# Kernel optimization log

Hardware: AMD Instinct MI355X
Metric: run time of the kernel (lower is better)

Reference implementation:

```python
import jax, jax.numpy as jnp
from jax import lax
import numpy as np

# ---- init hyperparameters (from init_kwargs) ----
STRIDE = 1
DP_CHANNELS = 1
ATOM_R = 8
ATOM_C = 8
NUMB_ATOM = 128
T_SC = 3
K = 256
BATCH = 32
IMG = 64


def setup_inputs() -> dict:
    key = jax.random.key(0)
    k1, k2 = jax.random.split(key)
    Y = jax.random.normal(k1, (BATCH, DP_CHANNELS, IMG, IMG), dtype=jnp.float32)
    # ConvTranspose2d weight layout: (numb_atom, dp_channels, atom_c, atom_r)
    W = jax.random.normal(k2, (NUMB_ATOM, DP_CHANNELS, ATOM_C, ATOM_R), dtype=jnp.float32)
    # normalise_weights(): each (i, j) filter divided by its L2 norm
    W = W / jnp.sqrt(jnp.sum(W ** 2, axis=(2, 3), keepdims=True))
    return {"Y": Y, "W_D": W}


def _conv_D(X, W):
    # PyTorch ConvTranspose2d (stride=1, no padding): full convolution with
    # spatially-flipped kernel; W is (in=numb_atom, out=dp_channels, kh, kw).
    kh, kw = W.shape[2], W.shape[3]
    return lax.conv_general_dilated(
        X, jnp.flip(W, (2, 3)), (1, 1),
        [(kh - 1, kh - 1), (kw - 1, kw - 1)],
        dimension_numbers=('NCHW', 'IOHW', 'NCHW'))


def _conv_Dt(R, Wt):
    # PyTorch Conv2d (VALID, stride=1): Wt is (out=numb_atom, in=dp, kh, kw)
    return lax.conv_general_dilated(
        R, Wt, (1, 1), 'VALID', dimension_numbers=('NCHW', 'OIHW', 'NCHW'))


def _hard_threshold_k(X, k):
    # keep the k largest-|.| entries per sample (over flattened C,H,W)
    B = X.shape[0]
    flat = X.reshape(B, -1)
    _, idx = lax.top_k(jnp.abs(flat), k)                      # [B, k]
    vals = jnp.take_along_axis(flat, idx, axis=1)             # [B, k]
    out = jnp.zeros_like(flat).at[jnp.arange(B)[:, None], idx].set(vals)
    return out.reshape(X.shape)


def _linesearch(Y, X, W, Wt, k):
    R = Y - _conv_D(X, W)
    g = _conv_Dt(R, Wt)
    l2_start = jnp.sum(R ** 2)

    def attempt(alpha):
        Xu = _hard_threshold_k(X + alpha * g, k)
        err = jnp.sum((Y - _conv_D(Xu, W)) ** 2)
        return Xu, err

    Xu0, err0 = attempt(jnp.float32(1.0))

    def cond(s):
        _, _, err, count = s
        return (err >= l2_start) & (count <= 15)

    def body(s):
        alpha, _, _, count = s
        alpha = alpha * jnp.float32(0.5)
        Xu, err = attempt(alpha)
        return (alpha, Xu, err, count + 1)

    alpha, Xu, err, _ = lax.while_loop(
        cond, body, (jnp.float32(1.0), Xu0, err0, jnp.int32(0)))
    return Xu, err, alpha


def reference(Y, W_D):
    # D_trans.weight = D.weight.permute(0,1,3,2) -> (numb_atom, dp, atom_r, atom_c)
    Wt = jnp.swapaxes(W_D, 2, 3)
    kh, kw = Wt.shape[2], Wt.shape[3]
    B, _, H, W_sp = Y.shape
    X = jnp.zeros((B, W_D.shape[0], H - kh + 1, W_sp - kw + 1), dtype=Y.dtype)
    for _ in range(T_SC):
        X, _, _ = _linesearch(Y, X, W_D, Wt, K)
    return X
```

## Files before the change

### kernel.cpp

```cpp
#include <hip/hip_runtime.h>
#include <stdint.h>

#define NB   32
#define NCH  128
#define IMG  64
#define IMG2 4096
#define OH   57
#define OHW  3249
#define CHW  415872
#define KTOP 256
#define NATT 17
#define NS   32
#define SCAP 512
#define NCAP 1536
#define NBUCK 8192
#define HSHIFT 18
#define TGT  512
#define RSTRIDE 72
#define NZB  257
#define BMW  12996

typedef unsigned long long ull;

__global__ void k_init(int* support_cnt) {
    if (threadIdx.x < NB) support_cnt[threadIdx.x] = 0;
}

__global__ __launch_bounds__(256) void k_resid(
    const float* __restrict__ Y, const float* __restrict__ W,
    const int* __restrict__ support_cnt, const uint32_t* __restrict__ support_idx,
    const float* __restrict__ support_val, float* __restrict__ Rg, double* __restrict__ l2part,
    uint32_t* __restrict__ hist, int* __restrict__ cand_cnt)
{
    int bx = blockIdx.x, tid = threadIdx.x;
    if (bx >= NB) {
        int zb = bx - NB;
        if (zb < 256) {
            ((uint4*)hist)[zb * 256 + tid] = make_uint4(0u, 0u, 0u, 0u);
        } else {
            ((uint4*)cand_cnt)[tid] = make_uint4(0u, 0u, 0u, 0u);
        }
        return;
    }
    int b = bx;
    __shared__ float Rs[IMG2];
    const float4* Y4 = (const float4*)(Y + b * IMG2);
    float4* R4 = (float4*)Rs;
    for (int i = tid; i < IMG2 / 4; i += 256) R4[i] = Y4[i];
    __syncthreads();
    int n = support_cnt[b];
    for (int task = tid; task < n * 64; task += 256) {
        int i = task >> 6, tap = task & 63, p = tap >> 3, q = tap & 7;
        uint32_t idx = support_idx[b * KTOP + i];
        float val = support_val[b * KTOP + i];
        int c = idx / OHW, rem = idx % OHW, s = rem / OH, t = rem % OH;
        float w = W[c * 64 + p * 8 + q];
        atomicAdd(&Rs[(s + p) * IMG + (t + q)], -val * w);
    }
    __syncthreads();
    double acc = 0.0;
    for (int i = tid; i < IMG2; i += 256) {
        float v = Rs[i];
        Rg[b * IMG2 + i] = v;
        acc += (double)v * (double)v;
    }
    __shared__ double red[256];
    red[tid] = acc; __syncthreads();
    for (int s2 = 128; s2 > 0; s2 >>= 1) { if (tid < s2) red[tid] += red[tid + s2]; __syncthreads(); }
    if (tid == 0) l2part[b] = red[0];
}

__global__ __launch_bounds__(256) void k_conv(
    const float* __restrict__ Rg, const float* __restrict__ W,
    float* __restrict__ g_out, uint32_t* __restrict__ hist)
{
    int b = blockIdx.x, cg0 = blockIdx.y, tid = threadIdx.x;
    __shared__ float Rs[71 * 72];
    __shared__ uint32_t hl[NBUCK];
    for (int i = tid; i < 71 * 72; i += 256) Rs[i] = 0.f;
    for (int i = tid; i < NBUCK; i += 256) hl[i] = 0u;
    __syncthreads();
    const float4* R4 = (const float4*)(Rg + b * IMG2);
    for (int i = tid; i < 1024; i += 256) {
        int row = i >> 4, col4 = (i & 15) * 4;
        *(float4*)&Rs[row * 72 + col4] = R4[i];
    }
    __syncthreads();
    int csub = tid >> 7;
    int tile = tid & 127;
    bool active = tile < 120;
    int tr = active ? tile / 15 : 0;
    int tc = active ? tile % 15 : 0;
    int s0 = tr * 8, t0 = tc * 4;

    for (int sub = 0; sub < 4; ++sub) {
        int c = cg0 * 8 + sub * 2 + csub;
        int c_s = __builtin_amdgcn_readfirstlane(c);
        const float* Wc = W + c_s * 64;

        float acc[8][4];
#pragma unroll
        for (int r = 0; r < 8; ++r)
#pragma unroll
            for (int cc = 0; cc < 4; ++cc) acc[r][cc] = 0.f;

#pragma unroll
        for (int rho = 0; rho < 15; ++rho) {
            float rb[12];
            const float* rp = &Rs[(s0 + rho) * 72 + t0];
            *(float4*)&rb[0] = *(const float4*)rp;
            *(float4*)&rb[4] = *(const float4*)(rp + 4);
            *(float4*)&rb[8] = *(const float4*)(rp + 8);
#pragma unroll
            for (int r = 0; r < 8; ++r) {
                const int p = rho - r;
                if (p >= 0 && p < 8) {
#pragma unroll
                    for (int q = 0; q < 8; ++q) {
                        float wv = Wc[q * 8 + p];
#pragma unroll
                        for (int cc = 0; cc < 4; ++cc)
                            acc[r][cc] = fmaf(rb[cc + q], wv, acc[r][cc]);
                    }
                }
            }
        }
        if (active) {
            float* go = g_out + (size_t)(b * NCH + c) * OHW;
#pragma unroll
            for (int r = 0; r < 8; ++r) {
                int s = s0 + r;
                if (s < OH) {
#pragma unroll
                    for (int cc = 0; cc < 4; ++cc) {
                        int t = t0 + cc;
                        if (t < OH) {
                            float v = acc[r][cc];
                            go[s * OH + t] = v;
                            uint32_t bits = __float_as_uint(v) & 0x7fffffffu;
                            atomicAdd(&hl[bits >> HSHIFT], 1u);
                        }
                    }
                }
            }
        }
    }
    __syncthreads();
    for (int i = tid; i < NBUCK; i += 256) {
        uint32_t v = hl[i];
        if (v) atomicAdd(&hist[b * NBUCK + i], v);
    }
}

__global__ __launch_bounds__(256) void k_thresh(const uint32_t* __restrict__ hist,
                                                uint32_t* __restrict__ thr) {
    int b = blockIdx.x, tid = threadIdx.x;
    uint32_t h[32];
    uint32_t s = 0;
    const uint32_t* hb = hist + b * NBUCK + tid * 32;
#pragma unroll
    for (int k = 0; k < 32; ++k) { h[k] = hb[k]; s += h[k]; }
    __shared__ uint32_t buf[2][256];
    int cur = 0;
    buf[0][tid] = s;
    __syncthreads();
    for (int d = 1; d < 256; d <<= 1) {
        uint32_t v = buf[cur][tid];
        if (tid + d < 256) v += buf[cur][tid + d];
        buf[cur ^ 1][tid] = v;
        cur ^= 1;
        __syncthreads();
    }
    uint32_t sufme = buf[cur][tid];
    uint32_t base  = (tid < 255) ? buf[cur][tid + 1] : 0u;
    if (tid == 0 && buf[cur][0] < TGT) thr[b] = 0u;
    if (base < TGT && sufme >= TGT) {
        uint32_t acc = base; int bk = 0;
#pragma unroll
        for (int k = 31; k >= 0; --k) {
            acc += h[k];
            if (acc >= TGT) { bk = tid * 32 + k; break; }
        }
        thr[b] = (uint32_t)bk << HSHIFT;
    }
}

__global__ __launch_bounds__(256) void k_collect(
    const float* __restrict__ g, const uint32_t* __restrict__ thr,
    int* __restrict__ cand_cnt, uint32_t* __restrict__ cand_idx, float* __restrict__ cand_g)
{
    int b = blockIdx.y;
    int i4 = blockIdx.x * 256 + threadIdx.x;
    if (i4 >= CHW / 4) return;
    int slice = blockIdx.x & (NS - 1);
    uint32_t tb = thr[b];
    float4 v4 = ((const float4*)(g + (size_t)b * CHW))[i4];
    float vv[4] = { v4.x, v4.y, v4.z, v4.w };
#pragma unroll
    for (int k = 0; k < 4; ++k) {
        uint32_t bits = __float_as_uint(vv[k]) & 0x7fffffffu;
        if (bits >= tb) {
            int pos = atomicAdd(&cand_cnt[b * NS + slice], 1);
            if (pos < SCAP) {
                cand_idx[(b * NS + slice) * SCAP + pos] = (uint32_t)(i4 * 4 + k);
                cand_g[(b * NS + slice) * SCAP + pos] = vv[k];
            }
        }
    }
}

__global__ __launch_bounds__(1024) void k_suppg(
    const float* __restrict__ g,
    const int* __restrict__ support_cnt, const uint32_t* __restrict__ support_idx,
    const int* __restrict__ cand_cnt, const uint32_t* __restrict__ cand_idx,
    const float* __restrict__ cand_g,
    uint32_t* __restrict__ ns_idx, float* __restrict__ ns_g, uint32_t* __restrict__ ns_pk,
    float* __restrict__ sup_g, uint32_t* __restrict__ sup_pk)
{
    int b = blockIdx.x, tid = threadIdx.x, lane = tid & 63;
    __shared__ uint32_t bm[BMW];
    __shared__ int cnts[NS];
    __shared__ ull ck[NCAP];
    __shared__ float cg_l[NCAP];
    __shared__ int nns_sh;
    int n = support_cnt[b];
    for (int i = tid; i < BMW / 4; i += 1024) ((uint4*)bm)[i] = make_uint4(0u, 0u, 0u, 0u);
    if (tid < NS) cnts[tid] = min(cand_cnt[b * NS + tid], SCAP);
    if (tid == 0) nns_sh = 0;
    __syncthreads();
    if (tid < KTOP) {
        if (tid < n) {
            uint32_t idx = support_idx[b * KTOP + tid];
            atomicOr(&bm[idx >> 5], 1u << (idx & 31));
            float gv = g[(size_t)b * CHW + idx];
            sup_g[b * KTOP + tid] = gv;
            int c = idx / OHW, r = idx % OHW, s = r / OH, t = r % OH;
            sup_pk[b * KTOP + tid] = (uint32_t)((c << 12) | (s << 6) | t);
        } else {
            sup_g[b * KTOP + tid] = 0.f;
            sup_pk[b * KTOP + tid] = 0u;
        }
    }
    __syncthreads();
    for (int t0 = tid; t0 < NS * SCAP; t0 += 1024) {
        int s = t0 >> 9, j = t0 & (SCAP - 1);
        bool keep = false; uint32_t idx = 0; float gv = 0.f;
        if (j < cnts[s]) {
            idx = cand_idx[(b * NS + s) * SCAP + j];
            gv = cand_g[(b * NS + s) * SCAP + j];
            keep = ((bm[idx >> 5] >> (idx & 31)) & 1u) == 0u;
        }
        ull mk = __ballot(keep);
        if (mk) {
            int basep = 0;
            if (lane == 0) basep = atomicAdd(&nns_sh, (int)__popcll(mk));
            basep = __shfl(basep, 0, 64);
            if (keep) {
                int p = basep + (int)__popcll(mk & ((1ull << lane) - 1ull));
                if (p < NCAP) {
                    ck[p] = ((ull)(__float_as_uint(gv) & 0x7fffffffu) << 32) | (ull)(uint32_t)(~idx);
                    cg_l[p] = gv;
                }
            }
        }
    }
    __syncthreads();
    int nns = min(nns_sh, NCAP);
    int nns8 = (nns + 7) & ~7;
    for (int i = nns + tid; i < nns8; i += 1024) ck[i] = 0ull;
    __syncthreads();
    ull myk[2]; int myr[2];
#pragma unroll
    for (int q = 0; q < 2; ++q) { int i = tid + 1024 * q; myk[q] = (i < nns) ? ck[i] : 0ull; myr[q] = 0; }
    for (int j = 0; j < nns8; j += 8) {
        ull t0 = ck[j], t1 = ck[j+1], t2 = ck[j+2], t3 = ck[j+3];
        ull t4 = ck[j+4], t5 = ck[j+5], t6 = ck[j+6], t7 = ck[j+7];
#pragma unroll
        for (int q = 0; q < 2; ++q) {
            myr[q] += ((t0 > myk[q]) ? 1 : 0) + ((t1 > myk[q]) ? 1 : 0)
                    + ((t2 > myk[q]) ? 1 : 0) + ((t3 > myk[q]) ? 1 : 0)
                    + ((t4 > myk[q]) ? 1 : 0) + ((t5 > myk[q]) ? 1 : 0)
                    + ((t6 > myk[q]) ? 1 : 0) + ((t7 > myk[q]) ? 1 : 0);
        }
    }
#pragma unroll
    for (int q = 0; q < 2; ++q) {
        int i = tid + 1024 * q;
        if (i < nns && myr[q] < KTOP) {
            uint32_t idx = ~(uint32_t)myk[q];
            int r = myr[q];
            ns_idx[b * KTOP + r] = idx;
            ns_g[b * KTOP + r] = cg_l[i];
            int c = idx / OHW, rr = idx % OHW, s = rr / OH, t = rr % OH;
            ns_pk[b * KTOP + r] = (uint32_t)((c << 12) | (s << 6) | t);
        }
    }
}

__global__ __launch_bounds__(1024) void k_att2(
    const float* __restrict__ Y, const float* __restrict__ W,
    const int* __restrict__ support_cnt, const uint32_t* __restrict__ support_idx,
    const float* __restrict__ support_val,
    const float* __restrict__ sup_g, const uint32_t* __restrict__ sup_pk,
    const uint32_t* __restrict__ ns_idx, const float* __restrict__ ns_g,
    const uint32_t* __restrict__ ns_pk,
    uint32_t* __restrict__ sel_idx, float* __restrict__ sel_val, double* __restrict__ err)
{
    int a = blockIdx.x, b = blockIdx.y, tid = threadIdx.x;
    int lane = tid & 63, wid = tid >> 6;
    float alpha = ldexpf(1.f, -a);
    int n = support_cnt[b];

    __shared__ float Wlds[NCH * 64];
    __shared__ float recon[64 * RSTRIDE];
    __shared__ ull kA[KTOP];
    __shared__ ull kB[KTOP];
    __shared__ float s_v[KTOP];
    __shared__ uint32_t s_pk2[KTOP];
    __shared__ double redd[16];

    uint32_t nsi = 0, pk_ns = 0, spi = 0, pk_sup = 0;
    float v_ns = 0.f, v_sup = 0.f;
    ull k_ns = 0, k_sup = 0;
    if (wid < 4) {
        nsi = ns_idx[b * KTOP + tid];
        v_ns = alpha * ns_g[b * KTOP + tid];
        pk_ns = ns_pk[b * KTOP + tid];
        k_ns = ((ull)(__float_as_uint(v_ns) & 0x7fffffffu) << 32) | (ull)(uint32_t)(~nsi);
        kA[tid] = k_ns;
        if (tid < n) {
            spi = support_idx[b * KTOP + tid];
            v_sup = fmaf(alpha, sup_g[b * KTOP + tid], support_val[b * KTOP + tid]);
            pk_sup = sup_pk[b * KTOP + tid];
        } else {
            spi = (uint32_t)(CHW + tid);
            v_sup = 0.f; pk_sup = 0u;
        }
        k_sup = ((ull)(__float_as_uint(v_sup) & 0x7fffffffu) << 32) | (ull)(uint32_t)(~spi);
        kB[tid] = k_sup;
    }
    __syncthreads();

    if (wid < 4) {
        int cb_ns = 0, cb_sup = 0;
        for (int j = 0; j < KTOP; j += 8) {
            ull t0 = kB[j], t1 = kB[j+1], t2 = kB[j+2], t3 = kB[j+3];
            ull t4 = kB[j+4], t5 = kB[j+5], t6 = kB[j+6], t7 = kB[j+7];
            cb_ns  += ((t0 > k_ns) ? 1 : 0) + ((t1 > k_ns) ? 1 : 0)
                    + ((t2 > k_ns) ? 1 : 0) + ((t3 > k_ns) ? 1 : 0)
                    + ((t4 > k_ns) ? 1 : 0) + ((t5 > k_ns) ? 1 : 0)
                    + ((t6 > k_ns) ? 1 : 0) + ((t7 > k_ns) ? 1 : 0);
            cb_sup += ((t0 > k_sup) ? 1 : 0) + ((t1 > k_sup) ? 1 : 0)
                    + ((t2 > k_sup) ? 1 : 0) + ((t3 > k_sup) ? 1 : 0)
                    + ((t4 > k_sup) ? 1 : 0) + ((t5 > k_sup) ? 1 : 0)
                    + ((t6 > k_sup) ? 1 : 0) + ((t7 > k_sup) ? 1 : 0);
        }
        int rank_ns = tid + cb_ns;
        int lo = 0, hi = KTOP;
        while (lo < hi) { int mid = (lo + hi) >> 1; if (kA[mid] > k_sup) lo = mid + 1; else hi = mid; }
        int rank_sup = lo + cb_sup;
        size_t o = ((size_t)a * NB + b) * KTOP;
        if (rank_ns < KTOP) {
            s_v[rank_ns] = v_ns; s_pk2[rank_ns] = pk_ns;
            sel_idx[o + rank_ns] = nsi; sel_val[o + rank_ns] = v_ns;
        }
        if (rank_sup < KTOP) {
            s_v[rank_sup] = v_sup; s_pk2[rank_sup] = pk_sup;
            sel_idx[o + rank_sup] = spi; sel_val[o + rank_sup] = v_sup;
        }
    } else {
        for (int i = tid - 256; i < 64 * RSTRIDE; i += 768) recon[i] = 0.f;
        for (int i = tid - 256; i < (NCH * 64) / 4; i += 768)
            ((float4*)Wlds)[i] = ((const float4*)W)[i];
    }
    __syncthreads();

    for (int task = tid; task < KTOP * 64; task += 1024) {
        int i = task >> 6, tap = task & 63, p = tap >> 3, q = tap & 7;
        uint32_t pk = s_pk2[i];
        float val = s_v[i];
        int c = pk >> 12, s = (pk >> 6) & 63, t = pk & 63;
        atomicAdd(&recon[(s + p) * RSTRIDE + (t + q)], val * Wlds[c * 64 + tap]);
    }
    __syncthreads();

    float4 y4 = ((const float4*)(Y + b * IMG2))[tid];
    int row = tid >> 4, col = (tid & 15) * 4;
    const float* rr = &recon[row * RSTRIDE + col];
    double accd = 0.0;
    float d0 = y4.x - rr[0]; accd += (double)d0 * (double)d0;
    float d1 = y4.y - rr[1]; accd += (double)d1 * (double)d1;
    float d2 = y4.z - rr[2]; accd += (double)d2 * (double)d2;
    float d3 = y4.w - rr[3]; accd += (double)d3 * (double)d3;
    for (int d = 32; d > 0; d >>= 1) accd += __shfl_xor(accd, d, 64);
    if (lane == 0) redd[wid] = accd;
    __syncthreads();
    if (tid == 0) {
        double e = 0.0;
#pragma unroll
        for (int w2 = 0; w2 < 16; ++w2) e += redd[w2];
        err[a * NB + b] = e;
    }
}

__global__ __launch_bounds__(256) void k_update(
    const double* __restrict__ l2part, const double* __restrict__ err,
    const uint32_t* __restrict__ sel_idx, const float* __restrict__ sel_val,
    int* __restrict__ support_cnt, uint32_t* __restrict__ support_idx, float* __restrict__ support_val)
{
    int b = blockIdx.x, tid = threadIdx.x;
    __shared__ double esum[NATT + 1];
    __shared__ int sel_sh;
    if (tid < NATT) {
        double e = 0.0;
        for (int b2 = 0; b2 < NB; ++b2) e += err[tid * NB + b2];
        esum[tid] = e;
    } else if (tid == NATT) {
        double l2 = 0.0;
        for (int b2 = 0; b2 < NB; ++b2) l2 += l2part[b2];
        esum[NATT] = l2;
    }
    __syncthreads();
    if (tid == 0) {
        double l2 = esum[NATT];
        int sel = NATT - 1;
        for (int a2 = 0; a2 < NATT; ++a2) if (esum[a2] < l2) { sel = a2; break; }
        sel_sh = sel;
    }
    __syncthreads();
    int a = sel_sh;
    __shared__ uint32_t ki[KTOP];
    __shared__ float kv[KTOP];
    ki[tid] = sel_idx[((size_t)a * NB + b) * KTOP + tid];
    kv[tid] = sel_val[((size_t)a * NB + b) * KTOP + tid];
    __syncthreads();
    uint32_t me = ki[tid];
    int rank = 0;
    for (int j = 0; j < KTOP; j += 8) {
        uint32_t a0 = ki[j], a1 = ki[j+1], a2 = ki[j+2], a3 = ki[j+3];
        uint32_t a4 = ki[j+4], a5 = ki[j+5], a6 = ki[j+6], a7 = ki[j+7];
        rank += ((a0 < me) ? 1 : 0) + ((a1 < me) ? 1 : 0) + ((a2 < me) ? 1 : 0) + ((a3 < me) ? 1 : 0)
              + ((a4 < me) ? 1 : 0) + ((a5 < me) ? 1 : 0) + ((a6 < me) ? 1 : 0) + ((a7 < me) ? 1 : 0);
    }
    support_idx[b * KTOP + rank] = me;
    support_val[b * KTOP + rank] = kv[tid];
    if (tid == 0) support_cnt[b] = KTOP;
}

__global__ void k_outzero(float4* __restrict__ out) {
    int i = blockIdx.x * 256 + threadIdx.x;
    if (i < (NB * CHW) / 4) out[i] = make_float4(0.f, 0.f, 0.f, 0.f);
}

__global__ void k_scatter(const uint32_t* __restrict__ support_idx, const float* __restrict__ support_val,
                          float* __restrict__ out) {
    int b = blockIdx.x, tid = threadIdx.x;
    if (tid < KTOP) out[(size_t)b * CHW + support_idx[b * KTOP + tid]] = support_val[b * KTOP + tid];
}

static size_t align256(size_t x) { return (x + 255) & ~(size_t)255; }

extern "C" void kernel_launch(void* const* d_in, const int* in_sizes, int n_in,
                              void* d_out, int out_size, void* d_ws, size_t ws_size,
                              hipStream_t stream)
{
    const float* Y = (const float*)d_in[0];
    const float* W = (const float*)d_in[1];
    float* out = (float*)d_out;

    char* p = (char*)d_ws;
    size_t off = 0;
    auto carve = [&](size_t bytes) { void* r = p + off; off = align256(off + bytes); return r; };
    float*    Rg          = (float*)   carve(NB * IMG2 * sizeof(float));
    uint32_t* hist        = (uint32_t*)carve((size_t)NB * NBUCK * sizeof(uint32_t));
    uint32_t* thr         = (uint32_t*)carve(NB * sizeof(uint32_t));
    int*      cand_cnt    = (int*)     carve(NB * NS * sizeof(int));
    double*   l2part      = (double*)  carve(NB * sizeof(double));
    double*   err         = (double*)  carve(NATT * NB * sizeof(double));
    int*      support_cnt = (int*)     carve(NB * sizeof(int));
    uint32_t* support_idx = (uint32_t*)carve(NB * KTOP * sizeof(uint32_t));
    float*    support_val = (float*)   carve(NB * KTOP * sizeof(float));
    uint32_t* sel_idx     = (uint32_t*)carve((size_t)NATT * NB * KTOP * sizeof(uint32_t));
    float*    sel_val     = (float*)   carve((size_t)NATT * NB * KTOP * sizeof(float));
    uint32_t* cand_idx    = (uint32_t*)carve((size_t)NB * NS * SCAP * sizeof(uint32_t));
    float*    cand_g      = (float*)   carve((size_t)NB * NS * SCAP * sizeof(float));
    uint32_t* ns_idx      = (uint32_t*)carve(NB * KTOP * sizeof(uint32_t));
    float*    ns_gbuf     = (float*)   carve(NB * KTOP * sizeof(float));
    uint32_t* ns_pk       = (uint32_t*)carve(NB * KTOP * sizeof(uint32_t));
    float*    sup_gbuf    = (float*)   carve(NB * KTOP * sizeof(float));
    uint32_t* sup_pk      = (uint32_t*)carve(NB * KTOP * sizeof(uint32_t));
    (void)ws_size; (void)in_sizes; (void)n_in; (void)out_size;

    k_init<<<1, 64, 0, stream>>>(support_cnt);
    for (int t = 0; t < 3; ++t) {
        k_resid<<<NB + NZB, 256, 0, stream>>>(Y, W, support_cnt, support_idx, support_val,
                                              Rg, l2part, hist, cand_cnt);
        k_conv<<<dim3(NB, 16), 256, 0, stream>>>(Rg, W, out, hist);
        k_thresh<<<NB, 256, 0, stream>>>(hist, thr);
        k_collect<<<dim3((CHW / 4 + 255) / 256, NB), 256, 0, stream>>>(out, thr, cand_cnt, cand_idx, cand_g);
        k_suppg<<<NB, 1024, 0, stream>>>(out, support_cnt, support_idx,
                                         cand_cnt, cand_idx, cand_g,
                                         ns_idx, ns_gbuf, ns_pk, sup_gbuf, sup_pk);
        k_att2<<<dim3(NATT, NB), 1024, 0, stream>>>(Y, W, support_cnt, support_idx, support_val,
                                                    sup_gbuf, sup_pk, ns_idx, ns_gbuf, ns_pk,
                                                    sel_idx, sel_val, err);
        k_update<<<NB, 256, 0, stream>>>(l2part, err, sel_idx, sel_val,
                                         support_cnt, support_idx, support_val);
    }
    k_outzero<<<((NB * CHW) / 4 + 255) / 256, 256, 0, stream>>>((float4*)out);
    k_scatter<<<NB, 256, 0, stream>>>(support_idx, support_val, out);
}
```

Baseline: 671.4 us.

## Shrink k_att2 to 512 threads, drop LDS weight copy, rebalance merge work

Restructures the attempt-evaluation kernel to 512 threads. Each thread now ranks one candidate: the first 256 take the new-support entries and the rest take the existing support entries, replacing the scheme where 4 waves each ranked two entries while the other waves idled. The 32KB shared-memory copy of the weights is removed and the scatter reads W straight from global memory (cached). This lowers LDS use and block size so more blocks can be resident per CU. The cost is that the atomic scatter and the final error reduction now run with half as many threads.

```diff
diff --git a/kernel.cpp b/kernel.cpp
--- a/kernel.cpp
+++ b/kernel.cpp
@@ -297,7 +297,7 @@
     }
 }
 
-__global__ __launch_bounds__(1024) void k_att2(
+__global__ __launch_bounds__(512) void k_att2(
     const float* __restrict__ Y, const float* __restrict__ W,
     const int* __restrict__ support_cnt, const uint32_t* __restrict__ support_idx,
     const float* __restrict__ support_val,
@@ -311,94 +311,92 @@
     float alpha = ldexpf(1.f, -a);
     int n = support_cnt[b];
 
-    __shared__ float Wlds[NCH * 64];
     __shared__ float recon[64 * RSTRIDE];
     __shared__ ull kA[KTOP];
     __shared__ ull kB[KTOP];
     __shared__ float s_v[KTOP];
     __shared__ uint32_t s_pk2[KTOP];
-    __shared__ double redd[16];
-
-    uint32_t nsi = 0, pk_ns = 0, spi = 0, pk_sup = 0;
-    float v_ns = 0.f, v_sup = 0.f;
-    ull k_ns = 0, k_sup = 0;
-    if (wid < 4) {
-        nsi = ns_idx[b * KTOP + tid];
-        v_ns = alpha * ns_g[b * KTOP + tid];
-        pk_ns = ns_pk[b * KTOP + tid];
-        k_ns = ((ull)(__float_as_uint(v_ns) & 0x7fffffffu) << 32) | (ull)(uint32_t)(~nsi);
-        kA[tid] = k_ns;
-        if (tid < n) {
-            spi = support_idx[b * KTOP + tid];
-            v_sup = fmaf(alpha, sup_g[b * KTOP + tid], support_val[b * KTOP + tid]);
-            pk_sup = sup_pk[b * KTOP + tid];
+    __shared__ double redd[8];
+
+    uint32_t myi = 0, mypk = 0;
+    float myv = 0.f;
+    ull myk = 0;
+    if (tid < KTOP) {
+        myi = ns_idx[b * KTOP + tid];
+        myv = alpha * ns_g[b * KTOP + tid];
+        mypk = ns_pk[b * KTOP + tid];
+        myk = ((ull)(__float_as_uint(myv) & 0x7fffffffu) << 32) | (ull)(uint32_t)(~myi);
+        kA[tid] = myk;
+    } else {
+        int t2 = tid - KTOP;
+        if (t2 < n) {
+            myi = support_idx[b * KTOP + t2];
+            myv = fmaf(alpha, sup_g[b * KTOP + t2], support_val[b * KTOP + t2]);
+            mypk = sup_pk[b * KTOP + t2];
         } else {
-            spi = (uint32_t)(CHW + tid);
-            v_sup = 0.f; pk_sup = 0u;
-        }
-        k_sup = ((ull)(__float_as_uint(v_sup) & 0x7fffffffu) << 32) | (ull)(uint32_t)(~spi);
-        kB[tid] = k_sup;
-    }
-    __syncthreads();
-
-    if (wid < 4) {
-        int cb_ns = 0, cb_sup = 0;
-        for (int j = 0; j < KTOP; j += 8) {
-            ull t0 = kB[j], t1 = kB[j+1], t2 = kB[j+2], t3 = kB[j+3];
-            ull t4 = kB[j+4], t5 = kB[j+5], t6 = kB[j+6], t7 = kB[j+7];
-            cb_ns  += ((t0 > k_ns) ? 1 : 0) + ((t1 > k_ns) ? 1 : 0)
-                    + ((t2 > k_ns) ? 1 : 0) + ((t3 > k_ns) ? 1 : 0)
-                    + ((t4 > k_ns) ? 1 : 0) + ((t5 > k_ns) ? 1 : 0)
-                    + ((t6 > k_ns) ? 1 : 0) + ((t7 > k_ns) ? 1 : 0);
-            cb_sup += ((t0 > k_sup) ? 1 : 0) + ((t1 > k_sup) ? 1 : 0)
-                    + ((t2 > k_sup) ? 1 : 0) + ((t3 > k_sup) ? 1 : 0)
-                    + ((t4 > k_sup) ? 1 : 0) + ((t5 > k_sup) ? 1 : 0)
-                    + ((t6 > k_sup) ? 1 : 0) + ((t7 > k_sup) ? 1 : 0);
-        }
-        int rank_ns = tid + cb_ns;
+            myi = (uint32_t)(CHW + t2);
+            myv = 0.f; mypk = 0u;
+        }
+        myk = ((ull)(__float_as_uint(myv) & 0x7fffffffu) << 32) | (ull)(uint32_t)(~myi);
+        kB[t2] = myk;
+    }
+    for (int i = tid; i < 64 * RSTRIDE; i += 512) recon[i] = 0.f;
+    __syncthreads();
+
+    int cb = 0;
+    for (int j = 0; j < KTOP; j += 8) {
+        ull t0 = kB[j], t1 = kB[j+1], t2 = kB[j+2], t3 = kB[j+3];
+        ull t4 = kB[j+4], t5 = kB[j+5], t6 = kB[j+6], t7 = kB[j+7];
+        cb += ((t0 > myk) ? 1 : 0) + ((t1 > myk) ? 1 : 0)
+            + ((t2 > myk) ? 1 : 0) + ((t3 > myk) ? 1 : 0)
+            + ((t4 > myk) ? 1 : 0) + ((t5 > myk) ? 1 : 0)
+            + ((t6 > myk) ? 1 : 0) + ((t7 > myk) ? 1 : 0);
+    }
+    int rank;
+    if (tid < KTOP) {
+        rank = tid + cb;
+    } else {
         int lo = 0, hi = KTOP;
-        while (lo < hi) { int mid = (lo + hi) >> 1; if (kA[mid] > k_sup) lo = mid + 1; else hi = mid; }
-        int rank_sup = lo + cb_sup;
-        size_t o = ((size_t)a * NB + b) * KTOP;
-        if (rank_ns < KTOP) {
-            s_v[rank_ns] = v_ns; s_pk2[rank_ns] = pk_ns;
-            sel_idx[o + rank_ns] = nsi; sel_val[o + rank_ns] = v_ns;
-        }
-        if (rank_sup < KTOP) {
-            s_v[rank_sup] = v_sup; s_pk2[rank_sup] = pk_sup;
-            sel_idx[o + rank_sup] = spi; sel_val[o + rank_sup] = v_sup;
-        }
-    } else {
-        for (int i = tid - 256; i < 64 * RSTRIDE; i += 768) recon[i] = 0.f;
-        for (int i = tid - 256; i < (NCH * 64) / 4; i += 768)
-            ((float4*)Wlds)[i] = ((const float4*)W)[i];
-    }
-    __syncthreads();
-
-    for (int task = tid; task < KTOP * 64; task += 1024) {
+        while (lo < hi) { int mid = (lo + hi) >> 1; if (kA[mid] > myk) lo = mid + 1; else hi = mid; }
+        rank = lo + cb;
+    }
+    size_t o = ((size_t)a * NB + b) * KTOP;
+    if (rank < KTOP) {
+        s_v[rank] = myv; s_pk2[rank] = mypk;
+        sel_idx[o + rank] = myi; sel_val[o + rank] = myv;
+    }
+    __syncthreads();
+
+#pragma unroll 4
+    for (int task = tid; task < KTOP * 64; task += 512) {
         int i = task >> 6, tap = task & 63, p = tap >> 3, q = tap & 7;
         uint32_t pk = s_pk2[i];
         float val = s_v[i];
         int c = pk >> 12, s = (pk >> 6) & 63, t = pk & 63;
-        atomicAdd(&recon[(s + p) * RSTRIDE + (t + q)], val * Wlds[c * 64 + tap]);
-    }
-    __syncthreads();
-
-    float4 y4 = ((const float4*)(Y + b * IMG2))[tid];
-    int row = tid >> 4, col = (tid & 15) * 4;
-    const float* rr = &recon[row * RSTRIDE + col];
+        atomicAdd(&recon[(s + p) * RSTRIDE + (t + q)], val * W[c * 64 + tap]);
+    }
+    __syncthreads();
+
+    const float4* Y4 = (const float4*)(Y + b * IMG2);
     double accd = 0.0;
-    float d0 = y4.x - rr[0]; accd += (double)d0 * (double)d0;
-    float d1 = y4.y - rr[1]; accd += (double)d1 * (double)d1;
-    float d2 = y4.z - rr[2]; accd += (double)d2 * (double)d2;
-    float d3 = y4.w - rr[3]; accd += (double)d3 * (double)d3;
+#pragma unroll
+    for (int q2 = 0; q2 < 2; ++q2) {
+        int idx = tid * 2 + q2;
+        float4 y4 = Y4[idx];
+        int row = idx >> 4, col = (idx & 15) * 4;
+        const float* rr = &recon[row * RSTRIDE + col];
+        float d0 = y4.x - rr[0]; accd += (double)d0 * (double)d0;
+        float d1 = y4.y - rr[1]; accd += (double)d1 * (double)d1;
+        float d2 = y4.z - rr[2]; accd += (double)d2 * (double)d2;
+        float d3 = y4.w - rr[3]; accd += (double)d3 * (double)d3;
+    }
     for (int d = 32; d > 0; d >>= 1) accd += __shfl_xor(accd, d, 64);
     if (lane == 0) redd[wid] = accd;
     __syncthreads();
     if (tid == 0) {
         double e = 0.0;
 #pragma unroll
-        for (int w2 = 0; w2 < 16; ++w2) e += redd[w2];
+        for (int w2 = 0; w2 < 8; ++w2) e += redd[w2];
         err[a * NB + b] = e;
     }
 }
@@ -501,9 +499,9 @@
         k_suppg<<<NB, 1024, 0, stream>>>(out, support_cnt, support_idx,
                                          cand_cnt, cand_idx, cand_g,
                                          ns_idx, ns_gbuf, ns_pk, sup_gbuf, sup_pk);
-        k_att2<<<dim3(NATT, NB), 1024, 0, stream>>>(Y, W, support_cnt, support_idx, support_val,
-                                                    sup_gbuf, sup_pk, ns_idx, ns_gbuf, ns_pk,
-                                                    sel_idx, sel_val, err);
+        k_att2<<<dim3(NATT, NB), 512, 0, stream>>>(Y, W, support_cnt, support_idx, support_val,
+                                                   sup_gbuf, sup_pk, ns_idx, ns_gbuf, ns_pk,
+                                                   sel_idx, sel_val, err);
         k_update<<<NB, 256, 0, stream>>>(l2part, err, sel_idx, sel_val,
                                          support_cnt, support_idx, support_val);
     }
```

Result: no change. 663.3 us (-1.2%).
